# Kernel tuning notes

Hardware: AMD Instinct MI355X
Metric: run time of the kernel (lower is better)

Reference implementation:

```python
import jax, jax.numpy as jnp
import numpy as np

NUM_HEADS = 12
HEAD_DIM = 128
DIM = NUM_HEADS * HEAD_DIM  # 1536
ROTARY_DIM = HEAD_DIM       # partial_rotary_factor = 1
BASE = 10000.0
EPS = 1e-6


def rms_norm(x, scale):
    # RMSNorm over the full inner dim (applied before head split), Flux-style QKNorm
    var = jnp.mean(x * x, axis=-1, keepdims=True)
    return x * jax.lax.rsqrt(var + EPS) * scale


def rope_cos_sin(n):
    half = ROTARY_DIM // 2
    inv_freq = 1.0 / (BASE ** (jnp.arange(0, half, dtype=jnp.float32) / half))
    ang = jnp.arange(n, dtype=jnp.float32)[:, None] * inv_freq[None, :]  # [n, half]
    # broadcast over [b, n, h, half]
    return jnp.cos(ang)[None, :, None, :], jnp.sin(ang)[None, :, None, :]


def apply_rope(x, cos, sin):
    # x: [b, n, h, d]; rotate first ROTARY_DIM dims (NeoX half-split)
    half = ROTARY_DIM // 2
    x1 = x[..., :half]
    x2 = x[..., half:ROTARY_DIM]
    rest = x[..., ROTARY_DIM:]
    out = jnp.concatenate([x1 * cos - x2 * sin, x2 * cos + x1 * sin], axis=-1)
    if rest.shape[-1]:
        out = jnp.concatenate([out, rest], axis=-1)
    return out


def setup_inputs() -> dict:
    key = jax.random.key(0)
    ks = jax.random.split(key, 12)
    b, s_in, s_ctx = 2, 2048, 256
    sd = 0.02
    return {
        "input": jax.random.normal(ks[0], (b, s_in, DIM), dtype=jnp.float32),
        "context": jax.random.normal(ks[1], (b, s_ctx, DIM), dtype=jnp.float32),
        "W_qkv_in": jax.random.normal(ks[2], (DIM, 3 * DIM), dtype=jnp.float32) * sd,
        "b_qkv_in": jnp.zeros((3 * DIM,), dtype=jnp.float32),
        "W_qkv_ctx": jax.random.normal(ks[3], (DIM, 3 * DIM), dtype=jnp.float32) * sd,
        "b_qkv_ctx": jnp.zeros((3 * DIM,), dtype=jnp.float32),
        "qs_in": jnp.ones((DIM,), dtype=jnp.float32),
        "ks_in": jnp.ones((DIM,), dtype=jnp.float32),
        "qs_ctx": jnp.ones((DIM,), dtype=jnp.float32),
        "ks_ctx": jnp.ones((DIM,), dtype=jnp.float32),
        "W_out_in": jax.random.normal(ks[4], (DIM, DIM), dtype=jnp.float32) * sd,
        "b_out_in": jnp.zeros((DIM,), dtype=jnp.float32),
        "W_out_ctx": jax.random.normal(ks[5], (DIM, DIM), dtype=jnp.float32) * sd,
        "b_out_ctx": jnp.zeros((DIM,), dtype=jnp.float32),
    }


def reference(input, context, W_qkv_in, b_qkv_in, W_qkv_ctx, b_qkv_ctx,
              qs_in, ks_in, qs_ctx, ks_ctx,
              W_out_in, b_out_in, W_out_ctx, b_out_ctx):
    b = input.shape[0]
    s_ctx = context.shape[1]

    qi, ki, vi = jnp.split(input @ W_qkv_in + b_qkv_in, 3, axis=-1)
    qc, kc, vc = jnp.split(context @ W_qkv_ctx + b_qkv_ctx, 3, axis=-1)

    qi = rms_norm(qi, qs_in)
    ki = rms_norm(ki, ks_in)
    qc = rms_norm(qc, qs_ctx)
    kc = rms_norm(kc, ks_ctx)

    # concatenated joint sequence: context first, then input
    q = jnp.concatenate([qc, qi], axis=1)
    k = jnp.concatenate([kc, ki], axis=1)
    v = jnp.concatenate([vc, vi], axis=1)
    n = q.shape[1]

    q = q.reshape(b, n, NUM_HEADS, HEAD_DIM)
    k = k.reshape(b, n, NUM_HEADS, HEAD_DIM)
    v = v.reshape(b, n, NUM_HEADS, HEAD_DIM)

    cos, sin = rope_cos_sin(n)
    q = apply_rope(q, cos, sin)
    k = apply_rope(k, cos, sin)

    scale = HEAD_DIM ** -0.5
    attn = jnp.einsum("bqhd,bkhd->bhqk", q, k) * scale
    attn = jax.nn.softmax(attn, axis=-1)
    out = jnp.einsum("bhqk,bkhd->bqhd", attn, v).reshape(b, n, DIM)

    input_output = out[:, s_ctx:, :] @ W_out_in + b_out_in
    context_output = out[:, :s_ctx, :] @ W_out_ctx + b_out_ctx
    return (input_output, context_output)
```

## Files before the change

### kernel.cpp

```cpp
#include <hip/hip_runtime.h>
#include <hip/hip_bf16.h>

typedef __hip_bfloat16 bf16;
typedef __attribute__((ext_vector_type(8))) short short8;
typedef __attribute__((ext_vector_type(4))) float f32x4;

#define DIMC 1536
#define NQKV 4608
#define NH   12
#define HD   128
#define NTOK 2304
#define SCTX 256
#define SIN  2048
#define BATCH 2

__device__ __forceinline__ float bf2f(unsigned short u) {
    return __uint_as_float(((unsigned int)u) << 16);
}
__device__ __forceinline__ unsigned short f2bfu(float f) {
    bf16 h = (bf16)f; return *(unsigned short*)&h;
}

#define GLOAD16(gp, lp) __builtin_amdgcn_global_load_lds(                      \
    (__attribute__((address_space(1))) void*)(gp),                             \
    (__attribute__((address_space(3))) void*)(lp), 16, 0, 0)

__global__ __launch_bounds__(256) void cvt_both(
    const float* __restrict__ X0, unsigned short* __restrict__ Y0, int n4_0,
    const float* __restrict__ X1, unsigned short* __restrict__ Y1, int n4_1)
{
    int i = blockIdx.x * 256 + threadIdx.x;
    const float* X; unsigned short* Y;
    if (i < n4_0) { X = X0; Y = Y0; }
    else { i -= n4_0; if (i >= n4_1) return; X = X1; Y = Y1; }
    float4 v = ((const float4*)X)[i];
    union { unsigned short u[4]; uint2 p; } o;
    o.u[0] = f2bfu(v.x); o.u[1] = f2bfu(v.y);
    o.u[2] = f2bfu(v.z); o.u[3] = f2bfu(v.w);
    ((uint2*)Y)[i] = o.p;
}

__global__ __launch_bounds__(256) void transpose_cvt_pair(
    const float* __restrict__ W0, unsigned short* __restrict__ Wt0,
    const float* __restrict__ W1, unsigned short* __restrict__ Wt1,
    int K, int N)
{
    __shared__ float tile[32][33];
    const float* W = blockIdx.z ? W1 : W0;
    unsigned short* Wt = blockIdx.z ? Wt1 : Wt0;
    int n0 = blockIdx.x * 32, k0 = blockIdx.y * 32;
    int tx = threadIdx.x & 31, ty = threadIdx.x >> 5;
    #pragma unroll
    for (int i = 0; i < 4; ++i) {
        int kk = ty + i * 8;
        tile[kk][tx] = W[(size_t)(k0 + kk) * N + n0 + tx];
    }
    __syncthreads();
    #pragma unroll
    for (int i = 0; i < 4; ++i) {
        int nn = ty + i * 8;
        Wt[(size_t)(n0 + nn) * K + k0 + tx] = f2bfu(tile[tx][nn]);
    }
}

__global__ __launch_bounds__(256) void rope_table(
    float* __restrict__ cost, float* __restrict__ sint)
{
    int idx = blockIdx.x * 256 + threadIdx.x;
    if (idx >= NTOK * 64) return;
    int p = idx >> 6, j = idx & 63;
    float inv_freq = powf(10000.0f, -(float)j * (1.0f / 64.0f));
    float ang = (float)p * inv_freq;
    float sn, cs;
    sincosf(ang, &sn, &cs);
    cost[idx] = cs; sint[idx] = sn;
}

__device__ __forceinline__ void storeC(float* p, float v) { *p = v; }
__device__ __forceinline__ void storeC(unsigned short* p, float v) { *p = f2bfu(v); }

template <typename CT>
__global__ __launch_bounds__(256) void gemm_mfma(
    const unsigned short* __restrict__ A, const unsigned short* __restrict__ Wt,
    const float* __restrict__ bias, CT* __restrict__ C,
    int N, int K, int S, int aStr, int aOff, int cStr, int cOff)
{
    __shared__ __align__(16) unsigned short a_lds[128 * 32];
    __shared__ __align__(16) unsigned short b_lds[128 * 32];

    int tid = threadIdx.x;
    int wv = tid >> 6, lane = tid & 63;
    int wm = wv >> 1, wn = wv & 1;
    int quad = lane >> 4, l16 = lane & 15;
    int bm = blockIdx.y * 128, bn = blockIdx.x * 128;

    int m0 = tid >> 2;
    int c  = (tid & 3) ^ ((m0 >> 1) & 3);
    int r0 = bm + m0, r1 = bm + m0 + 64;
    size_t apA0 = ((size_t)((r0 / S) * aStr + aOff + (r0 % S))) * (size_t)K + c * 8;
    size_t apA1 = ((size_t)((r1 / S) * aStr + aOff + (r1 % S))) * (size_t)K + c * 8;
    size_t apB0 = (size_t)(bn + m0) * K + c * 8;
    size_t apB1 = (size_t)(bn + m0 + 64) * K + c * 8;

    unsigned short* ldsA0 = &a_lds[(wv * 64) * 8];
    unsigned short* ldsA1 = &a_lds[(256 + wv * 64) * 8];
    unsigned short* ldsB0 = &b_lds[(wv * 64) * 8];
    unsigned short* ldsB1 = &b_lds[(256 + wv * 64) * 8];

    int gA[4], gB[4];
    #pragma unroll
    for (int mt = 0; mt < 4; ++mt) {
        int m = wm * 64 + mt * 16 + l16;
        gA[mt] = (m * 4 + (quad ^ ((m >> 1) & 3))) * 8;
    }
    #pragma unroll
    for (int nt = 0; nt < 4; ++nt) {
        int n = wn * 64 + nt * 16 + l16;
        gB[nt] = (n * 4 + (quad ^ ((n >> 1) & 3))) * 8;
    }

    f32x4 acc[4][4];
    #pragma unroll
    for (int mt = 0; mt < 4; ++mt)
        #pragma unroll
        for (int nt = 0; nt < 4; ++nt) acc[mt][nt] = (f32x4){0.f, 0.f, 0.f, 0.f};

    for (int k0 = 0; k0 < K; k0 += 32) {
        GLOAD16(A + apA0 + k0, ldsA0);
        GLOAD16(A + apA1 + k0, ldsA1);
        GLOAD16(Wt + apB0 + k0, ldsB0);
        GLOAD16(Wt + apB1 + k0, ldsB1);
        __syncthreads();

        short8 af[4], bfr[4];
        #pragma unroll
        for (int mt = 0; mt < 4; ++mt) af[mt] = *(const short8*)&a_lds[gA[mt]];
        #pragma unroll
        for (int nt = 0; nt < 4; ++nt) bfr[nt] = *(const short8*)&b_lds[gB[nt]];
        #pragma unroll
        for (int mt = 0; mt < 4; ++mt)
            #pragma unroll
            for (int nt = 0; nt < 4; ++nt)
                acc[mt][nt] = __builtin_amdgcn_mfma_f32_16x16x32_bf16(
                    af[mt], bfr[nt], acc[mt][nt], 0, 0, 0);
        __syncthreads();
    }

    float bv[4];
    #pragma unroll
    for (int nt = 0; nt < 4; ++nt) bv[nt] = bias[bn + wn * 64 + nt * 16 + l16];
    #pragma unroll
    for (int mt = 0; mt < 4; ++mt) {
        #pragma unroll
        for (int r = 0; r < 4; ++r) {
            int row = bm + wm * 64 + mt * 16 + quad * 4 + r;
            size_t crow = (size_t)((row / S) * cStr + cOff + (row % S));
            CT* cp = C + crow * (size_t)N + bn + wn * 64 + l16;
            #pragma unroll
            for (int nt = 0; nt < 4; ++nt)
                storeC(cp + nt * 16, acc[mt][nt][r] + bv[nt]);
        }
    }
}

__global__ __launch_bounds__(256) void rms_rope_pack(
    const unsigned short* __restrict__ QKV,
    const float* __restrict__ qs_in, const float* __restrict__ ks_in,
    const float* __restrict__ qs_ctx, const float* __restrict__ ks_ctx,
    const float* __restrict__ cost, const float* __restrict__ sint,
    bf16* __restrict__ Q, bf16* __restrict__ K)
{
    __shared__ float qrow[DIMC];
    __shared__ float krow[DIMC];
    __shared__ float rq[4], rk[4];

    int token = blockIdx.x;
    int b = token / NTOK;
    int p = token % NTOK;
    bool is_ctx = (p < SCTX);
    const float* qs = is_ctx ? qs_ctx : qs_in;
    const float* ks = is_ctx ? ks_ctx : ks_in;

    int t = threadIdx.x;
    const unsigned short* row = QKV + (size_t)token * NQKV;

    float ssq_q = 0.f, ssq_k = 0.f;
    #pragma unroll
    for (int i = 0; i < 6; ++i) {
        int c = t + 256 * i;
        float q = bf2f(row[c]);
        float k = bf2f(row[DIMC + c]);
        qrow[c] = q; krow[c] = k;
        ssq_q += q * q; ssq_k += k * k;
    }
    for (int o = 32; o > 0; o >>= 1) {
        ssq_q += __shfl_down(ssq_q, o);
        ssq_k += __shfl_down(ssq_k, o);
    }
    if ((t & 63) == 0) { rq[t >> 6] = ssq_q; rk[t >> 6] = ssq_k; }
    __syncthreads();
    float sq = rq[0] + rq[1] + rq[2] + rq[3];
    float sk = rk[0] + rk[1] + rk[2] + rk[3];
    float invq = rsqrtf(sq * (1.0f / DIMC) + 1e-6f);
    float invk = rsqrtf(sk * (1.0f / DIMC) + 1e-6f);

    #pragma unroll
    for (int i = 0; i < 6; ++i) {
        int c = t + 256 * i;
        int d = c & 127;
        int j = d & 63;
        float cs = cost[p * 64 + j];
        float sn = sint[p * 64 + j];
        int pc = (d < 64) ? (c + 64) : (c - 64);

        float self_q = qrow[c]  * invq * qs[c];
        float part_q = qrow[pc] * invq * qs[pc];
        float qo = (d < 64) ? (self_q * cs - part_q * sn)
                            : (self_q * cs + part_q * sn);

        float self_k = krow[c]  * invk * ks[c];
        float part_k = krow[pc] * invk * ks[pc];
        float ko = (d < 64) ? (self_k * cs - part_k * sn)
                            : (self_k * cs + part_k * sn);

        int h = c >> 7;
        size_t qi = ((size_t)(b * NH + h) * NTOK + p) * HD + d;
        Q[qi] = (bf16)qo;
        K[qi] = (bf16)ko;
    }
}

__global__ __launch_bounds__(256) void vt_pack(
    const unsigned short* __restrict__ QKV, unsigned short* __restrict__ Vt)
{
    __shared__ unsigned short tileT[128][72];

    int pt = blockIdx.x % (NTOK / 64);
    int bh = blockIdx.x / (NTOK / 64);
    int b = bh / NH, h = bh % NH;
    int p0 = pt * 64;

    int t = threadIdx.x, wv = t >> 6, l = t & 63;

    const unsigned short* src =
        QKV + (size_t)(b * NTOK + p0 + l) * NQKV + 2 * DIMC + h * HD;
    #pragma unroll
    for (int it = 0; it < 4; ++it) {
        int c = it * 4 + wv;
        short8 v = *(const short8*)(src + c * 8);
        const unsigned short* vp = (const unsigned short*)&v;
        #pragma unroll
        for (int i = 0; i < 8; ++i) tileT[c * 8 + i][l] = vp[i];
    }
    __syncthreads();

    int d = t >> 1, jh = (t & 1) * 32;
    unsigned short* dst = Vt + ((size_t)bh * HD + d) * NTOK + p0 + jh;
    #pragma unroll
    for (int k = 0; k < 4; ++k) {
        short8 v = *(const short8*)&tileT[d][jh + k * 8];
        *(short8*)(dst + k * 8) = v;
    }
}

__global__ __launch_bounds__(256, 3) void attn_mfma(
    const unsigned short* __restrict__ Qh,
    const unsigned short* __restrict__ Kh,
    const unsigned short* __restrict__ Vth,
    bf16* __restrict__ O)
{
    __shared__ __align__(16) unsigned short k_lds[64 * 128];
    __shared__ __align__(16) unsigned short v_lds[128 * 64];
    __shared__ __align__(16) unsigned short p_lds[4][16][72];
    __shared__ float bc[4][16];

    int tid = threadIdx.x;
    int wv = tid >> 6, lane = tid & 63;
    int quad = lane >> 4, l16 = lane & 15;

    int qt = blockIdx.x % (NTOK / 64);
    int bh = blockIdx.x / (NTOK / 64);
    int b = bh / NH, h = bh % NH;
    int qw = qt * 64 + wv * 16;

    const unsigned short* Kbh = Kh + (size_t)bh * NTOK * HD;
    const unsigned short* Vbh = Vth + (size_t)bh * HD * NTOK;

    short8 qf[4];
    {
        const unsigned short* qrow =
            Qh + ((size_t)bh * NTOK + qw + l16) * HD + quad * 8;
        #pragma unroll
        for (int dk = 0; dk < 4; ++dk) qf[dk] = *(const short8*)(qrow + dk * 32);
    }

    float m_r[4], l_r[4];
    f32x4 oac[8];
    #pragma unroll
    for (int r = 0; r < 4; ++r) { m_r[r] = -1e30f; l_r[r] = 0.f; }
    #pragma unroll
    for (int md = 0; md < 8; ++md) oac[md] = (f32x4){0.f, 0.f, 0.f, 0.f};

    const float cscale = 0.08838834764831845f * 1.44269504088896f;

    int jrowK = wv * 4 + (lane >> 4);
    int cK = (lane & 15) ^ jrowK;
    int dV = wv * 8 + (lane >> 3);
    int cV = (lane & 7) ^ (lane >> 3);

    for (int j0 = 0; j0 < NTOK; j0 += 64) {
        #pragma unroll
        for (int it = 0; it < 4; ++it)
            GLOAD16(Kbh + (size_t)(j0 + it * 16 + jrowK) * HD + cK * 8,
                    &k_lds[(it * 256 + wv * 64) * 8]);
        #pragma unroll
        for (int it = 0; it < 4; ++it)
            GLOAD16(Vbh + (size_t)(it * 32 + dV) * NTOK + j0 + cV * 8,
                    &v_lds[(it * 256 + wv * 64) * 8]);
        __syncthreads();

        f32x4 s[4];
        #pragma unroll
        for (int n = 0; n < 4; ++n) {
            int jl = n * 16 + l16;
            f32x4 a0 = (f32x4){0.f, 0.f, 0.f, 0.f};
            #pragma unroll
            for (int dk = 0; dk < 4; ++dk) {
                short8 kf = *(const short8*)&k_lds[(jl * 16 + ((dk * 4 + quad) ^ l16)) * 8];
                a0 = __builtin_amdgcn_mfma_f32_16x16x32_bf16(qf[dk], kf, a0, 0, 0, 0);
            }
            s[n] = a0;
        }

        float alpha[4], rs[4];
        #pragma unroll
        for (int r = 0; r < 4; ++r) {
            float t = fmaxf(fmaxf(s[0][r], s[1][r]), fmaxf(s[2][r], s[3][r]));
            t = fmaxf(t, __shfl_xor(t, 1));
            t = fmaxf(t, __shfl_xor(t, 2));
            t = fmaxf(t, __shfl_xor(t, 4));
            t = fmaxf(t, __shfl_xor(t, 8));
            float mn = fmaxf(m_r[r], t * cscale);
            alpha[r] = exp2f(m_r[r] - mn);
            m_r[r] = mn;
            rs[r] = 0.f;
        }

        #pragma unroll
        for (int n = 0; n < 4; ++n) {
            #pragma unroll
            for (int r = 0; r < 4; ++r) {
                float e = exp2f(s[n][r] * cscale - m_r[r]);
                rs[r] += e;
                p_lds[wv][quad * 4 + r][n * 16 + l16] = f2bfu(e);
            }
        }
        #pragma unroll
        for (int r = 0; r < 4; ++r) {
            float t = rs[r];
            t += __shfl_xor(t, 1);
            t += __shfl_xor(t, 2);
            t += __shfl_xor(t, 4);
            t += __shfl_xor(t, 8);
            l_r[r] = l_r[r] * alpha[r] + t;
        }

        if (l16 == 0) {
            #pragma unroll
            for (int r = 0; r < 4; ++r) bc[wv][quad * 4 + r] = alpha[r];
        }
        float al = bc[wv][l16];
        #pragma unroll
        for (int md = 0; md < 8; ++md) {
            oac[md][0] *= al; oac[md][1] *= al;
            oac[md][2] *= al; oac[md][3] *= al;
        }

        #pragma unroll
        for (int kt = 0; kt < 2; ++kt) {
            short8 pf = *(const short8*)&p_lds[wv][l16][kt * 32 + quad * 8];
            #pragma unroll
            for (int md = 0; md < 8; ++md) {
                int dl = md * 16 + l16;
                short8 vf = *(const short8*)&v_lds[(dl * 8 + ((kt * 4 + quad) ^ (l16 & 7))) * 8];
                oac[md] = __builtin_amdgcn_mfma_f32_16x16x32_bf16(vf, pf, oac[md], 0, 0, 0);
            }
        }
        __syncthreads();
    }

    if (l16 == 0) {
        #pragma unroll
        for (int r = 0; r < 4; ++r) bc[wv][quad * 4 + r] = l_r[r];
    }
    float il = 1.0f / bc[wv][l16];

    int q = qw + l16;
    unsigned short* obase = (unsigned short*)O +
        ((size_t)(b * NTOK) + q) * DIMC + h * HD + quad * 4;
    #pragma unroll
    for (int md = 0; md < 8; ++md) {
        union { unsigned short u[4]; uint2 v; } pk;
        #pragma unroll
        for (int r = 0; r < 4; ++r) pk.u[r] = f2bfu(oac[md][r] * il);
        *(uint2*)(obase + md * 16) = pk.v;
    }
}

extern "C" void kernel_launch(void* const* d_in, const int* in_sizes, int n_in,
                              void* d_out, int out_size, void* d_ws, size_t ws_size,
                              hipStream_t stream)
{
    const float* input     = (const float*)d_in[0];
    const float* context   = (const float*)d_in[1];
    const float* W_qkv_in  = (const float*)d_in[2];
    const float* b_qkv_in  = (const float*)d_in[3];
    const float* W_qkv_ctx = (const float*)d_in[4];
    const float* b_qkv_ctx = (const float*)d_in[5];
    const float* qs_in     = (const float*)d_in[6];
    const float* ks_in     = (const float*)d_in[7];
    const float* qs_ctx    = (const float*)d_in[8];
    const float* ks_ctx    = (const float*)d_in[9];
    const float* W_out_in  = (const float*)d_in[10];
    const float* b_out_in  = (const float*)d_in[11];
    const float* W_out_ctx = (const float*)d_in[12];
    const float* b_out_ctx = (const float*)d_in[13];
    float* out = (float*)d_out;

    char* ws = (char*)d_ws;
    unsigned short* QKVb = (unsigned short*)ws;
    bf16*           Ob   = (bf16*)ws;
    unsigned short* Qb   = (unsigned short*)(ws + 42467328);
    unsigned short* Kb   = Qb + (size_t)BATCH * NH * NTOK * HD;
    unsigned short* Vtb  = Kb + (size_t)BATCH * NH * NTOK * HD;
    unsigned short* AbIn  = (unsigned short*)(ws + 84934656);
    unsigned short* AbCtx = AbIn + (size_t)BATCH * SIN * DIMC;
    float* costab = (float*)(ws + 84934656);
    float* sintab = costab + NTOK * 64;
    unsigned short* WtOutIn  = (unsigned short*)(ws + 84934656);
    unsigned short* WtOutCtx = WtOutIn + (size_t)DIMC * DIMC;
    unsigned short* WtQkvIn  = (unsigned short*)(ws + 99090432);
    unsigned short* WtQkvCtx = (unsigned short*)(ws + 113246208);

    int n4in = BATCH * SIN * DIMC / 4, n4ctx = BATCH * SCTX * DIMC / 4;
    cvt_both<<<(n4in + n4ctx + 255) / 256, 256, 0, stream>>>(
        input, AbIn, n4in, context, AbCtx, n4ctx);
    transpose_cvt_pair<<<dim3(NQKV / 32, DIMC / 32, 2), 256, 0, stream>>>(
        W_qkv_in, WtQkvIn, W_qkv_ctx, WtQkvCtx, DIMC, NQKV);

    gemm_mfma<unsigned short><<<dim3(NQKV / 128, (BATCH * SIN) / 128), 256, 0, stream>>>(
        AbIn, WtQkvIn, b_qkv_in, QKVb, NQKV, DIMC, SIN, SIN, 0, NTOK, SCTX);
    gemm_mfma<unsigned short><<<dim3(NQKV / 128, (BATCH * SCTX) / 128), 256, 0, stream>>>(
        AbCtx, WtQkvCtx, b_qkv_ctx, QKVb, NQKV, DIMC, SCTX, SCTX, 0, NTOK, 0);

    rope_table<<<(NTOK * 64 + 255) / 256, 256, 0, stream>>>(costab, sintab);
    rms_rope_pack<<<BATCH * NTOK, 256, 0, stream>>>(
        QKVb, qs_in, ks_in, qs_ctx, ks_ctx, costab, sintab, (bf16*)Qb, (bf16*)Kb);
    vt_pack<<<BATCH * NH * (NTOK / 64), 256, 0, stream>>>(QKVb, Vtb);

    attn_mfma<<<BATCH * NH * (NTOK / 64), 256, 0, stream>>>(Qb, Kb, Vtb, Ob);

    transpose_cvt_pair<<<dim3(DIMC / 32, DIMC / 32, 2), 256, 0, stream>>>(
        W_out_in, WtOutIn, W_out_ctx, WtOutCtx, DIMC, DIMC);

    gemm_mfma<float><<<dim3(DIMC / 128, (BATCH * SIN) / 128), 256, 0, stream>>>(
        (const unsigned short*)Ob, WtOutIn, b_out_in, out,
        DIMC, DIMC, SIN, NTOK, SCTX, SIN, 0);
    gemm_mfma<float><<<dim3(DIMC / 128, (BATCH * SCTX) / 128), 256, 0, stream>>>(
        (const unsigned short*)Ob, WtOutCtx, b_out_ctx, out + (size_t)BATCH * SIN * DIMC,
        DIMC, DIMC, SCTX, NTOK, 0, SCTX, 0);
}
```

Measured before the change: 571.8 us.

## Split attention over KV halves with 128-query tiles and in-register softmax

The attention kernel now processes 128 queries per block (32 per wave), so each K/V tile loaded into LDS is reused across twice as many queries. The key sequence is split in two, with partial outputs and (max, sum) stats written to workspace and merged by a new combine kernel. S is computed transposed so the softmax reductions stay within lanes, and P is fed straight from registers into 16x16x16 MFMAs, removing the P round-trip through LDS. The cost is extra register pressure from doubled accumulators, extra global traffic for the bf16 partials, one more kernel launch, and a small precision loss from storing unnormalized partials in bf16.

```diff
diff --git a/kernel.cpp b/kernel.cpp
--- a/kernel.cpp
+++ b/kernel.cpp
@@ -3,6 +3,7 @@
 
 typedef __hip_bfloat16 bf16;
 typedef __attribute__((ext_vector_type(8))) short short8;
+typedef __attribute__((ext_vector_type(4))) short s4b;
 typedef __attribute__((ext_vector_type(4))) float f32x4;
 
 #define DIMC 1536
@@ -13,6 +14,8 @@
 #define SCTX 256
 #define SIN  2048
 #define BATCH 2
+#define KV_SPLIT 2
+#define KT_SPLIT (NTOK / 64 / KV_SPLIT)
 
 __device__ __forceinline__ float bf2f(unsigned short u) {
     return __uint_as_float(((unsigned int)u) << 16);
@@ -20,6 +23,16 @@
 __device__ __forceinline__ unsigned short f2bfu(float f) {
     bf16 h = (bf16)f; return *(unsigned short*)&h;
 }
+
+#if __has_builtin(__builtin_amdgcn_mfma_f32_16x16x16bf16_1k)
+#define HAVE_MFMA16 1
+#define MFMA16(a, b, c) __builtin_amdgcn_mfma_f32_16x16x16bf16_1k(a, b, c, 0, 0, 0)
+#elif __has_builtin(__builtin_amdgcn_mfma_f32_16x16x16_bf16)
+#define HAVE_MFMA16 1
+#define MFMA16(a, b, c) __builtin_amdgcn_mfma_f32_16x16x16_bf16(a, b, c, 0, 0, 0)
+#else
+#define HAVE_MFMA16 0
+#endif
 
 #define GLOAD16(gp, lp) __builtin_amdgcn_global_load_lds(                      \
     (__attribute__((address_space(1))) void*)(gp),                             \
@@ -267,39 +280,43 @@
     const unsigned short* __restrict__ Qh,
     const unsigned short* __restrict__ Kh,
     const unsigned short* __restrict__ Vth,
-    bf16* __restrict__ O)
+    unsigned short* __restrict__ PO,
+    float2* __restrict__ PL)
 {
     __shared__ __align__(16) unsigned short k_lds[64 * 128];
     __shared__ __align__(16) unsigned short v_lds[128 * 64];
-    __shared__ __align__(16) unsigned short p_lds[4][16][72];
-    __shared__ float bc[4][16];
+#if !HAVE_MFMA16
+    __shared__ __align__(16) unsigned short p_buf[4][2][2][64 * 8];
+#endif
 
     int tid = threadIdx.x;
     int wv = tid >> 6, lane = tid & 63;
     int quad = lane >> 4, l16 = lane & 15;
 
-    int qt = blockIdx.x % (NTOK / 64);
-    int bh = blockIdx.x / (NTOK / 64);
-    int b = bh / NH, h = bh % NH;
-    int qw = qt * 64 + wv * 16;
+    int split = blockIdx.x & (KV_SPLIT - 1);
+    int rest  = blockIdx.x / KV_SPLIT;
+    int qt = rest % (NTOK / 128);
+    int bh = rest / (NTOK / 128);
+    int qw = qt * 128 + wv * 32;
 
     const unsigned short* Kbh = Kh + (size_t)bh * NTOK * HD;
     const unsigned short* Vbh = Vth + (size_t)bh * HD * NTOK;
 
-    short8 qf[4];
-    {
+    short8 qf[2][4];
+    #pragma unroll
+    for (int nsub = 0; nsub < 2; ++nsub) {
         const unsigned short* qrow =
-            Qh + ((size_t)bh * NTOK + qw + l16) * HD + quad * 8;
-        #pragma unroll
-        for (int dk = 0; dk < 4; ++dk) qf[dk] = *(const short8*)(qrow + dk * 32);
-    }
-
-    float m_r[4], l_r[4];
-    f32x4 oac[8];
-    #pragma unroll
-    for (int r = 0; r < 4; ++r) { m_r[r] = -1e30f; l_r[r] = 0.f; }
-    #pragma unroll
-    for (int md = 0; md < 8; ++md) oac[md] = (f32x4){0.f, 0.f, 0.f, 0.f};
+            Qh + ((size_t)bh * NTOK + qw + nsub * 16 + l16) * HD + quad * 8;
+        #pragma unroll
+        for (int dk = 0; dk < 4; ++dk) qf[nsub][dk] = *(const short8*)(qrow + dk * 32);
+    }
+
+    float m_r[2] = {-1e30f, -1e30f}, l_r[2] = {0.f, 0.f};
+    f32x4 oac[8][2];
+    #pragma unroll
+    for (int md = 0; md < 8; ++md)
+        #pragma unroll
+        for (int nsub = 0; nsub < 2; ++nsub) oac[md][nsub] = (f32x4){0.f, 0.f, 0.f, 0.f};
 
     const float cscale = 0.08838834764831845f * 1.44269504088896f;
 
@@ -308,7 +325,8 @@
     int dV = wv * 8 + (lane >> 3);
     int cV = (lane & 7) ^ (lane >> 3);
 
-    for (int j0 = 0; j0 < NTOK; j0 += 64) {
+    for (int t = 0; t < KT_SPLIT; ++t) {
+        int j0 = (split * KT_SPLIT + t) * 64;
         #pragma unroll
         for (int it = 0; it < 4; ++it)
             GLOAD16(Kbh + (size_t)(j0 + it * 16 + jrowK) * HD + cK * 8,
@@ -319,92 +337,147 @@
                     &v_lds[(it * 256 + wv * 64) * 8]);
         __syncthreads();
 
-        f32x4 s[4];
-        #pragma unroll
-        for (int n = 0; n < 4; ++n) {
-            int jl = n * 16 + l16;
+        f32x4 s[4][2];
+        #pragma unroll
+        for (int msub = 0; msub < 4; ++msub) {
             f32x4 a0 = (f32x4){0.f, 0.f, 0.f, 0.f};
+            f32x4 a1 = (f32x4){0.f, 0.f, 0.f, 0.f};
             #pragma unroll
             for (int dk = 0; dk < 4; ++dk) {
-                short8 kf = *(const short8*)&k_lds[(jl * 16 + ((dk * 4 + quad) ^ l16)) * 8];
-                a0 = __builtin_amdgcn_mfma_f32_16x16x32_bf16(qf[dk], kf, a0, 0, 0, 0);
+                int jrow = msub * 16 + l16;
+                short8 kf = *(const short8*)&k_lds[(jrow * 16 + ((dk * 4 + quad) ^ l16)) * 8];
+                a0 = __builtin_amdgcn_mfma_f32_16x16x32_bf16(kf, qf[0][dk], a0, 0, 0, 0);
+                a1 = __builtin_amdgcn_mfma_f32_16x16x32_bf16(kf, qf[1][dk], a1, 0, 0, 0);
             }
-            s[n] = a0;
-        }
-
-        float alpha[4], rs[4];
-        #pragma unroll
-        for (int r = 0; r < 4; ++r) {
-            float t = fmaxf(fmaxf(s[0][r], s[1][r]), fmaxf(s[2][r], s[3][r]));
-            t = fmaxf(t, __shfl_xor(t, 1));
-            t = fmaxf(t, __shfl_xor(t, 2));
-            t = fmaxf(t, __shfl_xor(t, 4));
-            t = fmaxf(t, __shfl_xor(t, 8));
-            float mn = fmaxf(m_r[r], t * cscale);
-            alpha[r] = exp2f(m_r[r] - mn);
-            m_r[r] = mn;
-            rs[r] = 0.f;
-        }
-
-        #pragma unroll
-        for (int n = 0; n < 4; ++n) {
-            #pragma unroll
-            for (int r = 0; r < 4; ++r) {
-                float e = exp2f(s[n][r] * cscale - m_r[r]);
-                rs[r] += e;
-                p_lds[wv][quad * 4 + r][n * 16 + l16] = f2bfu(e);
+            s[msub][0] = a0; s[msub][1] = a1;
+        }
+
+        float alpha[2];
+        s4b p4[4][2];
+        #pragma unroll
+        for (int nsub = 0; nsub < 2; ++nsub) {
+            float tmax = s[0][nsub][0];
+            #pragma unroll
+            for (int msub = 0; msub < 4; ++msub)
+                #pragma unroll
+                for (int r = 0; r < 4; ++r) tmax = fmaxf(tmax, s[msub][nsub][r]);
+            tmax = fmaxf(tmax, __shfl_xor(tmax, 16));
+            tmax = fmaxf(tmax, __shfl_xor(tmax, 32));
+            float mn = fmaxf(m_r[nsub], tmax * cscale);
+            alpha[nsub] = exp2f(m_r[nsub] - mn);
+            m_r[nsub] = mn;
+            float sum = 0.f;
+            #pragma unroll
+            for (int msub = 0; msub < 4; ++msub) {
+                #pragma unroll
+                for (int r = 0; r < 4; ++r) {
+                    float e = exp2f(s[msub][nsub][r] * cscale - mn);
+                    sum += e;
+                    p4[msub][nsub][r] = (short)f2bfu(e);
+                }
             }
-        }
-        #pragma unroll
-        for (int r = 0; r < 4; ++r) {
-            float t = rs[r];
-            t += __shfl_xor(t, 1);
-            t += __shfl_xor(t, 2);
-            t += __shfl_xor(t, 4);
-            t += __shfl_xor(t, 8);
-            l_r[r] = l_r[r] * alpha[r] + t;
-        }
-
-        if (l16 == 0) {
-            #pragma unroll
-            for (int r = 0; r < 4; ++r) bc[wv][quad * 4 + r] = alpha[r];
-        }
-        float al = bc[wv][l16];
-        #pragma unroll
-        for (int md = 0; md < 8; ++md) {
-            oac[md][0] *= al; oac[md][1] *= al;
-            oac[md][2] *= al; oac[md][3] *= al;
-        }
-
-        #pragma unroll
-        for (int kt = 0; kt < 2; ++kt) {
-            short8 pf = *(const short8*)&p_lds[wv][l16][kt * 32 + quad * 8];
+            sum += __shfl_xor(sum, 16);
+            sum += __shfl_xor(sum, 32);
+            l_r[nsub] = l_r[nsub] * alpha[nsub] + sum;
+        }
+
+        #pragma unroll
+        for (int md = 0; md < 8; ++md)
+            #pragma unroll
+            for (int nsub = 0; nsub < 2; ++nsub) {
+                oac[md][nsub][0] *= alpha[nsub]; oac[md][nsub][1] *= alpha[nsub];
+                oac[md][nsub][2] *= alpha[nsub]; oac[md][nsub][3] *= alpha[nsub];
+            }
+
+#if HAVE_MFMA16
+        #pragma unroll
+        for (int kstep = 0; kstep < 4; ++kstep) {
             #pragma unroll
             for (int md = 0; md < 8; ++md) {
-                int dl = md * 16 + l16;
-                short8 vf = *(const short8*)&v_lds[(dl * 8 + ((kt * 4 + quad) ^ (l16 & 7))) * 8];
-                oac[md] = __builtin_amdgcn_mfma_f32_16x16x32_bf16(vf, pf, oac[md], 0, 0, 0);
+                int d = md * 16 + l16;
+                s4b vA = *(const s4b*)&v_lds[(d * 8 + ((kstep * 2 + (quad >> 1)) ^ (d & 7))) * 8
+                                             + (quad & 1) * 4];
+                oac[md][0] = MFMA16(vA, p4[kstep][0], oac[md][0]);
+                oac[md][1] = MFMA16(vA, p4[kstep][1], oac[md][1]);
             }
         }
+#else
+        #pragma unroll
+        for (int nsub = 0; nsub < 2; ++nsub)
+            #pragma unroll
+            for (int msub = 0; msub < 4; ++msub)
+                #pragma unroll
+                for (int r = 0; r < 4; ++r) {
+                    int o = (msub & 1) * 16 + quad * 4 + r;
+                    p_buf[wv][nsub][msub >> 1][((o >> 3) * 16 + l16) * 8 + (o & 7)] =
+                        (unsigned short)p4[msub][nsub][r];
+                }
+        #pragma unroll
+        for (int ksub = 0; ksub < 2; ++ksub) {
+            short8 pf0 = *(const short8*)&p_buf[wv][0][ksub][lane * 8];
+            short8 pf1 = *(const short8*)&p_buf[wv][1][ksub][lane * 8];
+            #pragma unroll
+            for (int md = 0; md < 8; ++md) {
+                int d = md * 16 + l16;
+                short8 vf = *(const short8*)&v_lds[(d * 8 + ((ksub * 4 + quad) ^ (d & 7))) * 8];
+                oac[md][0] = __builtin_amdgcn_mfma_f32_16x16x32_bf16(vf, pf0, oac[md][0], 0, 0, 0);
+                oac[md][1] = __builtin_amdgcn_mfma_f32_16x16x32_bf16(vf, pf1, oac[md][1], 0, 0, 0);
+            }
+        }
+#endif
         __syncthreads();
     }
 
-    if (l16 == 0) {
-        #pragma unroll
-        for (int r = 0; r < 4; ++r) bc[wv][quad * 4 + r] = l_r[r];
-    }
-    float il = 1.0f / bc[wv][l16];
-
-    int q = qw + l16;
-    unsigned short* obase = (unsigned short*)O +
-        ((size_t)(b * NTOK) + q) * DIMC + h * HD + quad * 4;
-    #pragma unroll
-    for (int md = 0; md < 8; ++md) {
-        union { unsigned short u[4]; uint2 v; } pk;
-        #pragma unroll
-        for (int r = 0; r < 4; ++r) pk.u[r] = f2bfu(oac[md][r] * il);
-        *(uint2*)(obase + md * 16) = pk.v;
-    }
+    size_t pobase = ((size_t)split * (BATCH * NH) + bh) * NTOK * HD;
+    #pragma unroll
+    for (int md = 0; md < 8; ++md)
+        #pragma unroll
+        for (int nsub = 0; nsub < 2; ++nsub) {
+            int q = qw + nsub * 16 + l16;
+            union { unsigned short u[4]; uint2 v; } pk;
+            #pragma unroll
+            for (int r = 0; r < 4; ++r) pk.u[r] = f2bfu(oac[md][nsub][r]);
+            *(uint2*)(PO + pobase + (size_t)q * HD + md * 16 + quad * 4) = pk.v;
+        }
+    if (quad == 0) {
+        #pragma unroll
+        for (int nsub = 0; nsub < 2; ++nsub) {
+            int q = qw + nsub * 16 + l16;
+            PL[(size_t)split * (BATCH * NH * NTOK) + (size_t)bh * NTOK + q] =
+                make_float2(m_r[nsub], l_r[nsub]);
+        }
+    }
+}
+
+__global__ __launch_bounds__(256) void attn_combine(
+    const unsigned short* __restrict__ PO, const float2* __restrict__ PL,
+    unsigned short* __restrict__ Ob)
+{
+    int idx = blockIdx.x * 256 + threadIdx.x;
+    if (idx >= BATCH * NH * NTOK * (HD / 4)) return;
+    int qlin = idx >> 5;
+    int dpos = (idx & 31) * 4;
+
+    float2 ml0 = PL[qlin];
+    float2 ml1 = PL[(size_t)(BATCH * NH * NTOK) + qlin];
+    float m = fmaxf(ml0.x, ml1.x);
+    float w0 = exp2f(ml0.x - m), w1 = exp2f(ml1.x - m);
+    float inv = 1.0f / (ml0.y * w0 + ml1.y * w1);
+
+    const size_t stride = (size_t)BATCH * NH * NTOK * HD;
+    size_t off = (size_t)qlin * HD + dpos;
+    uint2 a = *(const uint2*)(PO + off);
+    uint2 b2 = *(const uint2*)(PO + stride + off);
+    const unsigned short* au = (const unsigned short*)&a;
+    const unsigned short* bu = (const unsigned short*)&b2;
+    union { unsigned short u[4]; uint2 v; } pk;
+    #pragma unroll
+    for (int r = 0; r < 4; ++r)
+        pk.u[r] = f2bfu((bf2f(au[r]) * w0 + bf2f(bu[r]) * w1) * inv);
+
+    int bh = qlin / NTOK, q = qlin % NTOK;
+    int b = bh / NH, h = bh % NH;
+    *(uint2*)(Ob + ((size_t)(b * NTOK) + q) * DIMC + h * HD + dpos) = pk.v;
 }
 
 extern "C" void kernel_launch(void* const* d_in, const int* in_sizes, int n_in,
@@ -429,7 +502,8 @@
 
     char* ws = (char*)d_ws;
     unsigned short* QKVb = (unsigned short*)ws;
-    bf16*           Ob   = (bf16*)ws;
+    unsigned short* Ob   = (unsigned short*)ws;
+    unsigned short* PO   = (unsigned short*)(ws + 14155776);
     unsigned short* Qb   = (unsigned short*)(ws + 42467328);
     unsigned short* Kb   = Qb + (size_t)BATCH * NH * NTOK * HD;
     unsigned short* Vtb  = Kb + (size_t)BATCH * NH * NTOK * HD;
@@ -437,6 +511,7 @@
     unsigned short* AbCtx = AbIn + (size_t)BATCH * SIN * DIMC;
     float* costab = (float*)(ws + 84934656);
     float* sintab = costab + NTOK * 64;
+    float2* PL    = (float2*)(ws + 86114304);
     unsigned short* WtOutIn  = (unsigned short*)(ws + 84934656);
     unsigned short* WtOutCtx = WtOutIn + (size_t)DIMC * DIMC;
     unsigned short* WtQkvIn  = (unsigned short*)(ws + 99090432);
@@ -458,15 +533,18 @@
         QKVb, qs_in, ks_in, qs_ctx, ks_ctx, costab, sintab, (bf16*)Qb, (bf16*)Kb);
     vt_pack<<<BATCH * NH * (NTOK / 64), 256, 0, stream>>>(QKVb, Vtb);
 
-    attn_mfma<<<BATCH * NH * (NTOK / 64), 256, 0, stream>>>(Qb, Kb, Vtb, Ob);
+    attn_mfma<<<BATCH * NH * (NTOK / 128) * KV_SPLIT, 256, 0, stream>>>(
+        Qb, Kb, Vtb, PO, PL);
+    attn_combine<<<(BATCH * NH * NTOK * (HD / 4) + 255) / 256, 256, 0, stream>>>(
+        PO, PL, Ob);
 
     transpose_cvt_pair<<<dim3(DIMC / 32, DIMC / 32, 2), 256, 0, stream>>>(
         W_out_in, WtOutIn, W_out_ctx, WtOutCtx, DIMC, DIMC);
 
     gemm_mfma<float><<<dim3(DIMC / 128, (BATCH * SIN) / 128), 256, 0, stream>>>(
-        (const unsigned short*)Ob, WtOutIn, b_out_in, out,
+        Ob, WtOutIn, b_out_in, out,
         DIMC, DIMC, SIN, NTOK, SCTX, SIN, 0);
     gemm_mfma<float><<<dim3(DIMC / 128, (BATCH * SCTX) / 128), 256, 0, stream>>>(
-        (const unsigned short*)Ob, WtOutCtx, b_out_ctx, out + (size_t)BATCH * SIN * DIMC,
+        Ob, WtOutCtx, b_out_ctx, out + (size_t)BATCH * SIN * DIMC,
         DIMC, DIMC, SCTX, NTOK, 0, SCTX, 0);
 }
```

Measured after the change: 540.0 us. 5.6% less time.
